# Kernel optimization log

Hardware: AMD Instinct MI355X
Metric: run time of the kernel (lower is better)

Reference implementation:

```python
import jax, jax.numpy as jnp
import numpy as np

B, Hh, Ww, C, D = 32, 14, 14, 512, 8192

def setup_inputs() -> dict:
    key = jax.random.key(0)
    k1, k2, k3, k4, k5, k6 = jax.random.split(key, 6)
    bottom1 = jax.random.normal(k1, (B, Hh, Ww, C), dtype=jnp.float32)
    bottom2 = jax.random.normal(k2, (B, Hh, Ww, C), dtype=jnp.float32)
    # rand_s: random +/-1 (trainable weights in the original layer)
    rand_s_1 = (2.0 * jax.random.randint(k3, (C,), 0, 2).astype(jnp.float32) - 1.0)
    rand_s_2 = (2.0 * jax.random.randint(k4, (C,), 0, 2).astype(jnp.float32) - 1.0)
    # rand_h: hash bucket index in [0, D) per input channel (fixed, non-trainable)
    rand_h_1 = jax.random.randint(k5, (C,), 0, D, dtype=jnp.int32)
    rand_h_2 = jax.random.randint(k6, (C,), 0, D, dtype=jnp.int32)
    return {"bottom1": bottom1, "bottom2": bottom2,
            "rand_s_1": rand_s_1, "rand_s_2": rand_s_2,
            "rand_h_1": rand_h_1, "rand_h_2": rand_h_2}

def _count_sketch(x_flat, rand_s, rand_h, out_dim):
    # x_flat: [N, C]. Equivalent to x_flat @ sparse_sketch_matrix [C, out_dim]
    # where sketch[c, rand_h[c]] = rand_s[c].
    z = x_flat * rand_s                                   # [N, C]
    # scatter-add channels into their hash buckets along the feature axis
    return jax.ops.segment_sum(z.T, rand_h, num_segments=out_dim).T  # [N, D]

def reference(bottom1, bottom2, rand_s_1, rand_s_2, rand_h_1, rand_h_2):
    b, h, w, c1 = bottom1.shape
    c2 = bottom2.shape[-1]
    x1 = bottom1.reshape(-1, c1)
    x2 = bottom2.reshape(-1, c2)
    sk1 = _count_sketch(x1, rand_s_1, rand_h_1, D)        # [N, D]
    sk2 = _count_sketch(x2, rand_s_2, rand_h_2, D)        # [N, D]
    fft1 = jnp.fft.fft(sk1.astype(jnp.complex64), axis=-1)
    fft2 = jnp.fft.fft(sk2.astype(jnp.complex64), axis=-1)
    cbp_flat = jnp.real(jnp.fft.ifft(fft1 * fft2, axis=-1))  # circular conv
    cbp = cbp_flat.reshape(b, h, w, D)
    return jnp.sum(cbp, axis=(1, 2))                      # [B, D]
```

## Files before the change

### kernel.cpp

```cpp
#include <hip/hip_runtime.h>


#define NB   32
#define HW   196
#define CC   512
#define DD   8192
#define KP   224
#define NTHR 256
#define TILES_PER_B 16

typedef __attribute__((ext_vector_type(8)))  __bf16 bf8;
typedef __attribute__((ext_vector_type(16))) float  f32x16;

#define G_BYTES    ((size_t)NB * TILES_PER_B * 128 * 128 * 4)
#define XT_ELEMS   ((size_t)NB * CC * KP)
#define XT_BYTES   (XT_ELEMS * 2)
#define PART_BYTES ((size_t)NB * TILES_PER_B * DD * 4)
#define NEED_SPLIT (G_BYTES + PART_BYTES)
#define NEED_R5    PART_BYTES

__global__ __launch_bounds__(NTHR) void cbp_transpose_kernel(
    const float* __restrict__ x1, const float* __restrict__ x2,
    const float* __restrict__ s1, const float* __restrict__ s2,
    __bf16* __restrict__ xT1, __bf16* __restrict__ xT2)
{
    __shared__ float T[64][65];
    const int bid = blockIdx.x;
    const int b  = bid >> 5;
    const int ct = (bid >> 2) & 7;
    const int kt = bid & 3;
    const int tid = threadIdx.x;

    #pragma unroll
    for (int m = 0; m < 2; ++m) {
        const float* x   = m ? x2  : x1;
        const float* s   = m ? s2  : s1;
        __bf16*      xTo = m ? xT2 : xT1;

        #pragma unroll
        for (int p = 0; p < 4; ++p) {
            const int row  = p * 16 + (tid >> 4);
            const int col4 = (tid & 15) * 4;
            const int k = kt * 64 + row;
            float4 v = {0.f, 0.f, 0.f, 0.f};
            if (k < HW)
                v = *(const float4*)(x + ((size_t)(b * HW + k) * CC + ct * 64 + col4));
            T[col4 + 0][row] = v.x;
            T[col4 + 1][row] = v.y;
            T[col4 + 2][row] = v.z;
            T[col4 + 3][row] = v.w;
        }
        __syncthreads();

        const int c_l = tid >> 2;
        const int seg = tid & 3;
        const int kp0 = kt * 64 + seg * 16;
        if (kp0 < KP) {
            const float sv = s[ct * 64 + c_l];
            const size_t dstc = (size_t)(b * CC + ct * 64 + c_l) * KP;
            #pragma unroll
            for (int i2 = 0; i2 < 2; ++i2) {
                bf8 v;
                #pragma unroll
                for (int i = 0; i < 8; ++i)
                    v[i] = (__bf16)(T[c_l][seg * 16 + i2 * 8 + i] * sv);
                *(bf8*)(xTo + dstc + kp0 + i2 * 8) = v;
            }
        }
        __syncthreads();
    }
}

__global__ __launch_bounds__(NTHR, 5) void cbp_gram2_kernel(
    const __bf16* __restrict__ xT1, const __bf16* __restrict__ xT2,
    float* __restrict__ G)
{
    const int bid  = blockIdx.x;
    const int swz  = (bid & 7) * 256 + (bid >> 3);
    const int tid  = threadIdx.x;
    const int wid  = tid >> 6;
    const int lane = tid & 63;
    const int lo5  = lane & 31;
    const int hi   = lane >> 5;

    const int t  = swz * 4 + wid;
    const int b  = t >> 8;
    const int r  = t & 255;
    const int u1 = r >> 4;
    const int u2 = r & 15;

    const __bf16* A  = xT1 + ((size_t)(b * CC + u1 * 32 + lo5) * KP + hi * 8);
    const __bf16* Bp = xT2 + ((size_t)(b * CC + u2 * 32 + lo5) * KP + hi * 8);

    f32x16 acc = {};
    bf8 Af[7], Bf[7];

    #pragma unroll
    for (int s = 0; s < 7; ++s) {
        Af[s] = *(const bf8*)(A  + s * 16);
        Bf[s] = *(const bf8*)(Bp + s * 16);
    }
    #pragma unroll
    for (int s = 0; s < 7; ++s)
        acc = __builtin_amdgcn_mfma_f32_32x32x16_bf16(Af[s], Bf[s], acc, 0, 0, 0);

    #pragma unroll
    for (int s = 0; s < 7; ++s) {
        Af[s] = *(const bf8*)(A  + (7 + s) * 16);
        Bf[s] = *(const bf8*)(Bp + (7 + s) * 16);
    }
    #pragma unroll
    for (int s = 0; s < 7; ++s)
        acc = __builtin_amdgcn_mfma_f32_32x32x16_bf16(Af[s], Bf[s], acc, 0, 0, 0);

    float* Gt = G + (size_t)(b * 16 + (u1 >> 2) * 4 + (u2 >> 2)) * (128 * 128);
    const int c2l = (u2 & 3) * 32 + lo5;
    #pragma unroll
    for (int reg = 0; reg < 16; ++reg) {
        const int c1l = (u1 & 3) * 32 + (reg & 3) + 8 * (reg >> 2) + 4 * hi;
        Gt[c1l * 128 + c2l] = acc[reg];
    }
}

__global__ __launch_bounds__(NTHR) void cbp_scatter_kernel(
    const float* __restrict__ G,
    const int* __restrict__ h1, const int* __restrict__ h2,
    float* __restrict__ partials)
{
    __shared__ float accD[DD];
    __shared__ int   h1t[128];
    __shared__ int   h2t[128];

    const int bid = blockIdx.x;
    const int t1  = (bid >> 2) & 3;
    const int t2  = bid & 3;
    const int tid = threadIdx.x;

    if (tid < 128)      h1t[tid]       = h1[t1 * 128 + tid];
    else if (tid < 256) h2t[tid - 128] = h2[t2 * 128 + (tid - 128)];
    for (int i = tid; i < DD; i += NTHR) accD[i] = 0.0f;
    __syncthreads();

    const float4* Gt = (const float4*)(G + (size_t)bid * (128 * 128));
    #pragma unroll
    for (int i = 0; i < 16; ++i) {
        const int idx  = tid + i * NTHR;
        const int c1l  = idx >> 5;
        const int c2l4 = (idx & 31) * 4;
        const float4 v = Gt[idx];
        const int hb = h1t[c1l];
        unsafeAtomicAdd(&accD[(hb + h2t[c2l4 + 0]) & (DD - 1)], v.x);
        unsafeAtomicAdd(&accD[(hb + h2t[c2l4 + 1]) & (DD - 1)], v.y);
        unsafeAtomicAdd(&accD[(hb + h2t[c2l4 + 2]) & (DD - 1)], v.z);
        unsafeAtomicAdd(&accD[(hb + h2t[c2l4 + 3]) & (DD - 1)], v.w);
    }
    __syncthreads();

    float4* dst = (float4*)(partials + (size_t)bid * DD);
    const float4* src = (const float4*)accD;
    #pragma unroll
    for (int i = 0; i < DD / 4 / NTHR; ++i)
        dst[tid + i * NTHR] = src[tid + i * NTHR];
}

__global__ __launch_bounds__(NTHR) void cbp_reduce_kernel(
    const float* __restrict__ parts, float* __restrict__ out)
{
    const int b  = blockIdx.x >> 3;
    const int d0 = (blockIdx.x & 7) * 1024 + threadIdx.x * 4;
    const float* base = parts + (size_t)b * TILES_PER_B * DD + d0;
    float4 sum = {0.f, 0.f, 0.f, 0.f};
    #pragma unroll
    for (int t = 0; t < TILES_PER_B; ++t) {
        float4 v = *(const float4*)(base + (size_t)t * DD);
        sum.x += v.x; sum.y += v.y; sum.z += v.z; sum.w += v.w;
    }
    *(float4*)(out + (size_t)b * DD + d0) = sum;
}

__global__ __launch_bounds__(NTHR) void cbp_mfma_kernel(
    const float* __restrict__ x1, const float* __restrict__ x2,
    const float* __restrict__ s1, const float* __restrict__ s2,
    const int*   __restrict__ h1, const int*   __restrict__ h2,
    float* __restrict__ ws, float* __restrict__ out, int use_ws)
{
    __shared__ float accD[DD];
    const int bid  = blockIdx.x;
    const int b    = bid >> 4;
    const int t1   = (bid >> 2) & 3;
    const int t2   = bid & 3;
    const int tid  = threadIdx.x;
    const int wid  = tid >> 6;
    const int lane = tid & 63;
    const int wr   = wid >> 1;
    const int wc   = wid & 1;
    const int lo5  = lane & 31;
    const int hi   = lane >> 5;

    for (int i = tid; i < DD; i += NTHR) accD[i] = 0.0f;
    __syncthreads();

    const int c1w = t1 * 128 + wr * 64;
    const int c2w = t2 * 128 + wc * 64;
    const float* A0 = x1 + (size_t)b * HW * CC + (c1w + lo5);
    const float* A1 = A0 + 32;
    const float* B0 = x2 + (size_t)b * HW * CC + (c2w + lo5);
    const float* B1 = B0 + 32;

    f32x16 acc00 = {}, acc01 = {}, acc10 = {}, acc11 = {};
    for (int ks = 0; ks < 12; ++ks) {
        const int kb = ks * 16 + hi * 8;
        bf8 a0, a1, b0v, b1v;
        #pragma unroll
        for (int j = 0; j < 8; ++j) {
            const size_t off = (size_t)(kb + j) * CC;
            a0[j] = (__bf16)A0[off]; a1[j] = (__bf16)A1[off];
            b0v[j] = (__bf16)B0[off]; b1v[j] = (__bf16)B1[off];
        }
        acc00 = __builtin_amdgcn_mfma_f32_32x32x16_bf16(a0, b0v, acc00, 0, 0, 0);
        acc01 = __builtin_amdgcn_mfma_f32_32x32x16_bf16(a0, b1v, acc01, 0, 0, 0);
        acc10 = __builtin_amdgcn_mfma_f32_32x32x16_bf16(a1, b0v, acc10, 0, 0, 0);
        acc11 = __builtin_amdgcn_mfma_f32_32x32x16_bf16(a1, b1v, acc11, 0, 0, 0);
    }
    {
        const int kb = 192 + hi * 8;
        bf8 a0, a1, b0v, b1v;
        #pragma unroll
        for (int j = 0; j < 8; ++j) {
            const int k = kb + j;
            const size_t off = (size_t)k * CC;
            const bool v = (k < HW);
            a0[j]  = (__bf16)(v ? A0[off] : 0.0f);
            a1[j]  = (__bf16)(v ? A1[off] : 0.0f);
            b0v[j] = (__bf16)(v ? B0[off] : 0.0f);
            b1v[j] = (__bf16)(v ? B1[off] : 0.0f);
        }
        acc00 = __builtin_amdgcn_mfma_f32_32x32x16_bf16(a0, b0v, acc00, 0, 0, 0);
        acc01 = __builtin_amdgcn_mfma_f32_32x32x16_bf16(a0, b1v, acc01, 0, 0, 0);
        acc10 = __builtin_amdgcn_mfma_f32_32x32x16_bf16(a1, b0v, acc10, 0, 0, 0);
        acc11 = __builtin_amdgcn_mfma_f32_32x32x16_bf16(a1, b1v, acc11, 0, 0, 0);
    }

    const float s2v0 = s2[c2w + lo5];
    const float s2v1 = s2[c2w + 32 + lo5];
    const int   h2v0 = h2[c2w + lo5];
    const int   h2v1 = h2[c2w + 32 + lo5];
    #pragma unroll
    for (int rt = 0; rt < 2; ++rt) {
        const f32x16 accL = rt ? acc10 : acc00;
        const f32x16 accR = rt ? acc11 : acc01;
        #pragma unroll
        for (int reg = 0; reg < 16; ++reg) {
            const int c1 = c1w + rt * 32 + (reg & 3) + 8 * (reg >> 2) + 4 * hi;
            const float sv = s1[c1];
            const int   hv = h1[c1];
            unsafeAtomicAdd(&accD[(hv + h2v0) & (DD - 1)], sv * s2v0 * accL[reg]);
            unsafeAtomicAdd(&accD[(hv + h2v1) & (DD - 1)], sv * s2v1 * accR[reg]);
        }
    }
    __syncthreads();

    if (use_ws) {
        float4* dst = (float4*)(ws + (size_t)bid * DD);
        const float4* src = (const float4*)accD;
        #pragma unroll
        for (int i = 0; i < DD / 4 / NTHR; ++i)
            dst[tid + i * NTHR] = src[tid + i * NTHR];
    } else {
        float* ob = out + (size_t)b * DD;
        for (int i = tid; i < DD; i += NTHR)
            atomicAdd(&ob[i], accD[i]);
    }
}

extern "C" void kernel_launch(void* const* d_in, const int* in_sizes, int n_in,
                              void* d_out, int out_size, void* d_ws, size_t ws_size,
                              hipStream_t stream) {
    const float* x1 = (const float*)d_in[0];
    const float* x2 = (const float*)d_in[1];
    const float* s1 = (const float*)d_in[2];
    const float* s2 = (const float*)d_in[3];
    const int*   h1 = (const int*)d_in[4];
    const int*   h2 = (const int*)d_in[5];
    float* out = (float*)d_out;

    dim3 block(NTHR);
    if (ws_size >= NEED_SPLIT) {
        float*  G     = (float*)d_ws;
        __bf16* xT1   = (__bf16*)((char*)d_ws + G_BYTES);
        __bf16* xT2   = xT1 + XT_ELEMS;
        float*  parts = (float*)((char*)d_ws + G_BYTES);
        cbp_transpose_kernel<<<dim3(NB * 32), block, 0, stream>>>(
            x1, x2, s1, s2, xT1, xT2);
        cbp_gram2_kernel<<<dim3(2048), block, 0, stream>>>(xT1, xT2, G);
        cbp_scatter_kernel<<<dim3(NB * TILES_PER_B), block, 0, stream>>>(
            G, h1, h2, parts);
        cbp_reduce_kernel<<<dim3(NB * 8), block, 0, stream>>>(parts, out);
    } else if (ws_size >= NEED_R5) {
        float* parts = (float*)d_ws;
        cbp_mfma_kernel<<<dim3(NB * TILES_PER_B), block, 0, stream>>>(
            x1, x2, s1, s2, h1, h2, parts, out, 1);
        cbp_reduce_kernel<<<dim3(NB * 8), block, 0, stream>>>(parts, out);
    } else {
        hipMemsetAsync(out, 0, (size_t)out_size * sizeof(float), stream);
        cbp_mfma_kernel<<<dim3(NB * TILES_PER_B), block, 0, stream>>>(
            x1, x2, s1, s2, h1, h2, (float*)d_ws, out, 0);
    }
}
```

Baseline: 150.9 us.

## Replace atomic scatter of Gram tiles with bucket-sorted gather via pair lists

```diff
diff --git a/kernel.cpp b/kernel.cpp
--- a/kernel.cpp
+++ b/kernel.cpp
@@ -7,16 +7,24 @@
 #define DD   8192
 #define KP   224
 #define NTHR 256
+#define NPAIR (CC * CC)
 #define TILES_PER_B 16
 
 typedef __attribute__((ext_vector_type(8)))  __bf16 bf8;
 typedef __attribute__((ext_vector_type(16))) float  f32x16;
 
-#define G_BYTES    ((size_t)NB * TILES_PER_B * 128 * 128 * 4)
+#define G_BYTES    ((size_t)NB * CC * CC * 4)
 #define XT_ELEMS   ((size_t)NB * CC * KP)
 #define XT_BYTES   (XT_ELEMS * 2)
+#define OFF_G      ((size_t)0)
+#define OFF_XT1    (G_BYTES)
+#define OFF_XT2    (OFF_XT1 + XT_BYTES)
+#define OFF_CNT    (OFF_XT2 + XT_BYTES)
+#define OFF_CUR    (OFF_CNT + 32768)
+#define OFF_OFF    (OFF_CUR + 32768)
+#define OFF_LIST   (OFF_OFF + 32832)
+#define NEED_GATHER (OFF_LIST + (size_t)NPAIR * 4)
 #define PART_BYTES ((size_t)NB * TILES_PER_B * DD * 4)
-#define NEED_SPLIT (G_BYTES + PART_BYTES)
 #define NEED_R5    PART_BYTES
 
 __global__ __launch_bounds__(NTHR) void cbp_transpose_kernel(
@@ -71,7 +79,55 @@
     }
 }
 
-__global__ __launch_bounds__(NTHR, 5) void cbp_gram2_kernel(
+__global__ __launch_bounds__(NTHR) void cbp_hist_kernel(
+    const int* __restrict__ h1, const int* __restrict__ h2,
+    int* __restrict__ cnt)
+{
+    const int gtid = blockIdx.x * NTHR + threadIdx.x;
+    for (int i = gtid; i < NPAIR; i += 65536) {
+        const int bkt = (h1[i >> 9] + h2[i & 511]) & (DD - 1);
+        atomicAdd(&cnt[bkt], 1);
+    }
+}
+
+__global__ __launch_bounds__(NTHR) void cbp_scan_kernel(
+    const int* __restrict__ cnt, int* __restrict__ off)
+{
+    __shared__ int ls[NTHR];
+    const int tid  = threadIdx.x;
+    const int base = tid * 32;
+    int loc[32];
+    int s = 0;
+    #pragma unroll
+    for (int k = 0; k < 32; ++k) { loc[k] = s; s += cnt[base + k]; }
+    ls[tid] = s;
+    __syncthreads();
+    for (int d = 1; d < NTHR; d <<= 1) {
+        int v = (tid >= d) ? ls[tid - d] : 0;
+        __syncthreads();
+        ls[tid] += v;
+        __syncthreads();
+    }
+    const int blockbase = (tid == 0) ? 0 : ls[tid - 1];
+    #pragma unroll
+    for (int k = 0; k < 32; ++k) off[base + k] = blockbase + loc[k];
+    if (tid == NTHR - 1) off[DD] = ls[NTHR - 1];
+}
+
+__global__ __launch_bounds__(NTHR) void cbp_fill_kernel(
+    const int* __restrict__ h1, const int* __restrict__ h2,
+    const int* __restrict__ off, int* __restrict__ cursor,
+    unsigned int* __restrict__ list)
+{
+    const int gtid = blockIdx.x * NTHR + threadIdx.x;
+    for (int i = gtid; i < NPAIR; i += 65536) {
+        const int bkt = (h1[i >> 9] + h2[i & 511]) & (DD - 1);
+        const int pos = off[bkt] + atomicAdd(&cursor[bkt], 1);
+        list[pos] = (unsigned int)i;
+    }
+}
+
+__global__ __launch_bounds__(NTHR, 5) void cbp_gram_flat_kernel(
     const __bf16* __restrict__ xT1, const __bf16* __restrict__ xT2,
     float* __restrict__ G)
 {
@@ -113,69 +169,32 @@
     for (int s = 0; s < 7; ++s)
         acc = __builtin_amdgcn_mfma_f32_32x32x16_bf16(Af[s], Bf[s], acc, 0, 0, 0);
 
-    float* Gt = G + (size_t)(b * 16 + (u1 >> 2) * 4 + (u2 >> 2)) * (128 * 128);
-    const int c2l = (u2 & 3) * 32 + lo5;
+    float* Gb = G + (size_t)b * (CC * CC);
+    const int c2 = u2 * 32 + lo5;
     #pragma unroll
     for (int reg = 0; reg < 16; ++reg) {
-        const int c1l = (u1 & 3) * 32 + (reg & 3) + 8 * (reg >> 2) + 4 * hi;
-        Gt[c1l * 128 + c2l] = acc[reg];
-    }
-}
-
-__global__ __launch_bounds__(NTHR) void cbp_scatter_kernel(
-    const float* __restrict__ G,
-    const int* __restrict__ h1, const int* __restrict__ h2,
-    float* __restrict__ partials)
-{
-    __shared__ float accD[DD];
-    __shared__ int   h1t[128];
-    __shared__ int   h2t[128];
-
-    const int bid = blockIdx.x;
-    const int t1  = (bid >> 2) & 3;
-    const int t2  = bid & 3;
-    const int tid = threadIdx.x;
-
-    if (tid < 128)      h1t[tid]       = h1[t1 * 128 + tid];
-    else if (tid < 256) h2t[tid - 128] = h2[t2 * 128 + (tid - 128)];
-    for (int i = tid; i < DD; i += NTHR) accD[i] = 0.0f;
-    __syncthreads();
-
-    const float4* Gt = (const float4*)(G + (size_t)bid * (128 * 128));
-    #pragma unroll
-    for (int i = 0; i < 16; ++i) {
-        const int idx  = tid + i * NTHR;
-        const int c1l  = idx >> 5;
-        const int c2l4 = (idx & 31) * 4;
-        const float4 v = Gt[idx];
-        const int hb = h1t[c1l];
-        unsafeAtomicAdd(&accD[(hb + h2t[c2l4 + 0]) & (DD - 1)], v.x);
-        unsafeAtomicAdd(&accD[(hb + h2t[c2l4 + 1]) & (DD - 1)], v.y);
-        unsafeAtomicAdd(&accD[(hb + h2t[c2l4 + 2]) & (DD - 1)], v.z);
-        unsafeAtomicAdd(&accD[(hb + h2t[c2l4 + 3]) & (DD - 1)], v.w);
-    }
-    __syncthreads();
-
-    float4* dst = (float4*)(partials + (size_t)bid * DD);
-    const float4* src = (const float4*)accD;
-    #pragma unroll
-    for (int i = 0; i < DD / 4 / NTHR; ++i)
-        dst[tid + i * NTHR] = src[tid + i * NTHR];
-}
-
-__global__ __launch_bounds__(NTHR) void cbp_reduce_kernel(
-    const float* __restrict__ parts, float* __restrict__ out)
-{
-    const int b  = blockIdx.x >> 3;
-    const int d0 = (blockIdx.x & 7) * 1024 + threadIdx.x * 4;
-    const float* base = parts + (size_t)b * TILES_PER_B * DD + d0;
-    float4 sum = {0.f, 0.f, 0.f, 0.f};
-    #pragma unroll
-    for (int t = 0; t < TILES_PER_B; ++t) {
-        float4 v = *(const float4*)(base + (size_t)t * DD);
-        sum.x += v.x; sum.y += v.y; sum.z += v.z; sum.w += v.w;
-    }
-    *(float4*)(out + (size_t)b * DD + d0) = sum;
+        const int c1 = u1 * 32 + (reg & 3) + 8 * (reg >> 2) + 4 * hi;
+        Gb[c1 * CC + c2] = acc[reg];
+    }
+}
+
+__global__ __launch_bounds__(NTHR) void cbp_gather_kernel(
+    const float* __restrict__ G, const unsigned int* __restrict__ list,
+    const int* __restrict__ off, float* __restrict__ out)
+{
+    const int bid0 = blockIdx.x;
+    const int swz  = (bid0 & 7) * 128 + (bid0 >> 3);
+    const int b    = swz >> 5;
+    const int d    = (swz & 31) * 256 + threadIdx.x;
+
+    const int o1 = off[d];
+    const int o2 = off[d + 1];
+    const float* Gb = G + (size_t)b * (CC * CC);
+
+    float s = 0.0f;
+    for (int k = o1; k < o2; ++k)
+        s += Gb[list[k]];
+    out[(size_t)b * DD + d] = s;
 }
 
 __global__ __launch_bounds__(NTHR) void cbp_mfma_kernel(
@@ -213,9 +232,9 @@
         bf8 a0, a1, b0v, b1v;
         #pragma unroll
         for (int j = 0; j < 8; ++j) {
-            const size_t off = (size_t)(kb + j) * CC;
-            a0[j] = (__bf16)A0[off]; a1[j] = (__bf16)A1[off];
-            b0v[j] = (__bf16)B0[off]; b1v[j] = (__bf16)B1[off];
+            const size_t offx = (size_t)(kb + j) * CC;
+            a0[j] = (__bf16)A0[offx]; a1[j] = (__bf16)A1[offx];
+            b0v[j] = (__bf16)B0[offx]; b1v[j] = (__bf16)B1[offx];
         }
         acc00 = __builtin_amdgcn_mfma_f32_32x32x16_bf16(a0, b0v, acc00, 0, 0, 0);
         acc01 = __builtin_amdgcn_mfma_f32_32x32x16_bf16(a0, b1v, acc01, 0, 0, 0);
@@ -228,12 +247,12 @@
         #pragma unroll
         for (int j = 0; j < 8; ++j) {
             const int k = kb + j;
-            const size_t off = (size_t)k * CC;
+            const size_t offx = (size_t)k * CC;
             const bool v = (k < HW);
-            a0[j]  = (__bf16)(v ? A0[off] : 0.0f);
-            a1[j]  = (__bf16)(v ? A1[off] : 0.0f);
-            b0v[j] = (__bf16)(v ? B0[off] : 0.0f);
-            b1v[j] = (__bf16)(v ? B1[off] : 0.0f);
+            a0[j]  = (__bf16)(v ? A0[offx] : 0.0f);
+            a1[j]  = (__bf16)(v ? A1[offx] : 0.0f);
+            b0v[j] = (__bf16)(v ? B0[offx] : 0.0f);
+            b1v[j] = (__bf16)(v ? B1[offx] : 0.0f);
         }
         acc00 = __builtin_amdgcn_mfma_f32_32x32x16_bf16(a0, b0v, acc00, 0, 0, 0);
         acc01 = __builtin_amdgcn_mfma_f32_32x32x16_bf16(a0, b1v, acc01, 0, 0, 0);
@@ -271,6 +290,21 @@
         for (int i = tid; i < DD; i += NTHR)
             atomicAdd(&ob[i], accD[i]);
     }
+}
+
+__global__ __launch_bounds__(NTHR) void cbp_reduce_kernel(
+    const float* __restrict__ parts, float* __restrict__ out)
+{
+    const int b  = blockIdx.x >> 3;
+    const int d0 = (blockIdx.x & 7) * 1024 + threadIdx.x * 4;
+    const float* base = parts + (size_t)b * TILES_PER_B * DD + d0;
+    float4 sum = {0.f, 0.f, 0.f, 0.f};
+    #pragma unroll
+    for (int t = 0; t < TILES_PER_B; ++t) {
+        float4 v = *(const float4*)(base + (size_t)t * DD);
+        sum.x += v.x; sum.y += v.y; sum.z += v.z; sum.w += v.w;
+    }
+    *(float4*)(out + (size_t)b * DD + d0) = sum;
 }
 
 extern "C" void kernel_launch(void* const* d_in, const int* in_sizes, int n_in,
@@ -283,19 +317,27 @@
     const int*   h1 = (const int*)d_in[4];
     const int*   h2 = (const int*)d_in[5];
     float* out = (float*)d_out;
+    char*  ws  = (char*)d_ws;
 
     dim3 block(NTHR);
-    if (ws_size >= NEED_SPLIT) {
-        float*  G     = (float*)d_ws;
-        __bf16* xT1   = (__bf16*)((char*)d_ws + G_BYTES);
-        __bf16* xT2   = xT1 + XT_ELEMS;
-        float*  parts = (float*)((char*)d_ws + G_BYTES);
+    if (ws_size >= NEED_GATHER) {
+        float*        G      = (float*)(ws + OFF_G);
+        __bf16*       xT1    = (__bf16*)(ws + OFF_XT1);
+        __bf16*       xT2    = (__bf16*)(ws + OFF_XT2);
+        int*          cnt    = (int*)(ws + OFF_CNT);
+        int*          cursor = (int*)(ws + OFF_CUR);
+        int*          offb   = (int*)(ws + OFF_OFF);
+        unsigned int* list   = (unsigned int*)(ws + OFF_LIST);
+
+        hipMemsetAsync(cnt, 0, 65536, stream);
+
         cbp_transpose_kernel<<<dim3(NB * 32), block, 0, stream>>>(
             x1, x2, s1, s2, xT1, xT2);
-        cbp_gram2_kernel<<<dim3(2048), block, 0, stream>>>(xT1, xT2, G);
-        cbp_scatter_kernel<<<dim3(NB * TILES_PER_B), block, 0, stream>>>(
-            G, h1, h2, parts);
-        cbp_reduce_kernel<<<dim3(NB * 8), block, 0, stream>>>(parts, out);
+        cbp_hist_kernel<<<dim3(256), block, 0, stream>>>(h1, h2, cnt);
+        cbp_scan_kernel<<<dim3(1), block, 0, stream>>>(cnt, offb);
+        cbp_fill_kernel<<<dim3(256), block, 0, stream>>>(h1, h2, offb, cursor, list);
+        cbp_gram_flat_kernel<<<dim3(2048), block, 0, stream>>>(xT1, xT2, G);
+        cbp_gather_kernel<<<dim3(1024), block, 0, stream>>>(G, list, offb, out);
     } else if (ws_size >= NEED_R5) {
         float* parts = (float*)d_ws;
         cbp_mfma_kernel<<<dim3(NB * TILES_PER_B), block, 0, stream>>>(
```

Result: slower. 183.1 us (+21.4%).
